# Performance work log

Hardware: AMD Instinct MI355X
Metric: run time of the kernel (lower is better)

## Reference

```python
import jax, jax.numpy as jnp
import numpy as np

D_MODEL = 256
D_CLIP = 768
NHEAD = 8
HEAD_DIM = D_MODEL // NHEAD
Q_LEN = 100
B = 32
T_LEN = 1203


def setup_inputs() -> dict:
    key = jax.random.key(0)
    ks = jax.random.split(key, 16)
    xav = lambda k, o, i: jax.random.uniform(k, (o, i), jnp.float32, -1.0, 1.0) * np.sqrt(6.0 / (o + i))
    return {
        "tgt": jax.random.normal(ks[0], (Q_LEN, B, D_MODEL), jnp.float32),
        "text_classification": jax.random.normal(ks[1], (T_LEN, D_CLIP), jnp.float32),
        "query_pos": jax.random.normal(ks[2], (Q_LEN, B, D_MODEL), jnp.float32),
        "out_of_vocab_logits": jax.random.normal(ks[3], (B, Q_LEN, T_LEN), jnp.float32),
        "Wq": xav(ks[4], D_MODEL, D_MODEL), "bq": jnp.zeros((D_MODEL,), jnp.float32),
        "Wk": xav(ks[5], D_MODEL, D_CLIP), "bk": jnp.zeros((D_MODEL,), jnp.float32),
        "Wv": xav(ks[6], D_MODEL, D_CLIP), "bv": jnp.zeros((D_MODEL,), jnp.float32),
        "Wo": xav(ks[7], D_MODEL, D_MODEL), "bo": jnp.zeros((D_MODEL,), jnp.float32),
        "ln_g": jnp.ones((D_MODEL,), jnp.float32), "ln_b": jnp.zeros((D_MODEL,), jnp.float32),
        "logit_scale": jnp.asarray(np.log(1 / 0.07), jnp.float32),
    }


def _l2norm(x, eps=1e-6):
    # F.normalize: x / max(||x||, eps)
    n = jnp.sqrt(jnp.sum(x * x, axis=-1, keepdims=True))
    return x / jnp.maximum(n, eps)


def _layernorm(x, g, b, eps=1e-5):
    mu = jnp.mean(x, axis=-1, keepdims=True)
    var = jnp.mean((x - mu) ** 2, axis=-1, keepdims=True)
    return (x - mu) * jax.lax.rsqrt(var + eps) * g + b


def reference(tgt, text_classification, query_pos, out_of_vocab_logits,
              Wq, bq, Wk, bk, Wv, bv, Wo, bo, ln_g, ln_b, logit_scale):
    qin = tgt + query_pos                       # (Q, B, d_model)
    q = qin @ Wq.T + bq                         # (Q, B, d_model)
    # text embeddings shared across batch (2D path)
    k = text_classification @ Wk.T + bk         # (T, d_model)
    v = text_classification @ Wv.T + bv         # (T, d_model)

    q = q.transpose(1, 0, 2).reshape(B, Q_LEN, NHEAD, HEAD_DIM).transpose(0, 2, 1, 3)  # (B,h,Q,hd)
    k = k.reshape(T_LEN, NHEAD, HEAD_DIM).transpose(1, 0, 2)                            # (h,T,hd)
    v = v.reshape(T_LEN, NHEAD, HEAD_DIM).transpose(1, 0, 2)                            # (h,T,hd)

    q = _l2norm(q)
    k = _l2norm(k)
    scale = jnp.minimum(jnp.exp(logit_scale), 100.0)
    in_vocab = jnp.einsum('bhqd,hkd->bhqk', q, k) * scale                                # (B,h,Q,T)

    alpha = jnp.linspace(0.0, 1.0, NHEAD, dtype=in_vocab.dtype).reshape(1, NHEAD, 1, 1)
    logits = in_vocab * (1.0 - alpha) + out_of_vocab_logits[:, None] * alpha

    attn = jax.nn.softmax(logits, axis=-1)
    out = jnp.einsum('bhqk,hkd->bhqd', attn, v)                                          # (B,h,Q,hd)
    out = out.transpose(0, 2, 1, 3).reshape(B, Q_LEN, D_MODEL).transpose(1, 0, 2)        # (Q,B,d_model)
    out = out @ Wo.T + bo

    # forward_post: residual + layernorm (dropout=0)
    return _layernorm(tgt + out, ln_g, ln_b)
```

## Files before the change

### kernel.cpp

```cpp
#include <hip/hip_runtime.h>
#include <hip/hip_bf16.h>
#include <math.h>

#define D_MODEL 256
#define D_CLIP 768
#define NHEAD 8
#define HEAD_DIM 32
#define Q_LEN 100
#define BB 32
#define T_LEN 1203
#define TPAD 1216
#define MQ (Q_LEN*BB)
#define LOG2E 1.4426950408889634f

typedef __bf16 bf16_t;
typedef __bf16 bf16x8 __attribute__((ext_vector_type(8)));
typedef __bf16 bf16x4 __attribute__((ext_vector_type(4)));
typedef float f32x4 __attribute__((ext_vector_type(4)));

static __device__ __forceinline__ bf16_t to_bf16(float x) { return (bf16_t)x; }

__global__ void prep_kernel(const float* __restrict__ tgt, const float* __restrict__ qpos,
                            const float* __restrict__ text, const float* __restrict__ Wq,
                            const float* __restrict__ Wk, const float* __restrict__ Wv,
                            const float* __restrict__ Wo,
                            bf16_t* __restrict__ qin_bf, bf16_t* __restrict__ conv_dst) {
    int idx = blockIdx.x * 256 + threadIdx.x;
    if (idx >= 566848) return;
    float4 v;
    bf16_t* dst;
    if (idx < 204800) {
        float4 a = ((const float4*)tgt)[idx];
        float4 b = ((const float4*)qpos)[idx];
        v = make_float4(a.x + b.x, a.y + b.y, a.z + b.z, a.w + b.w);
        dst = qin_bf + idx * 4;
    } else {
        int j = idx - 204800;
        const float4* src;
        if (j < 230976)      src = (const float4*)text + j;
        else if (j < 247360) src = (const float4*)Wq + (j - 230976);
        else if (j < 296512) src = (const float4*)Wk + (j - 247360);
        else if (j < 345664) src = (const float4*)Wv + (j - 296512);
        else                 src = (const float4*)Wo + (j - 345664);
        v = *src;
        dst = conv_dst + (size_t)j * 4;
    }
    bf16x4 r = { to_bf16(v.x), to_bf16(v.y), to_bf16(v.z), to_bf16(v.w) };
    *(bf16x4*)dst = r;
}

__launch_bounds__(256)
__global__ void proj_kernel(const bf16_t* __restrict__ qin_bf, const bf16_t* __restrict__ text_bf,
                            const bf16_t* __restrict__ wq, const bf16_t* __restrict__ wk,
                            const bf16_t* __restrict__ wv,
                            const float* __restrict__ bq, const float* __restrict__ bk,
                            const float* __restrict__ bv,
                            bf16_t* __restrict__ qn, bf16_t* __restrict__ kn,
                            bf16_t* __restrict__ vT) {
    const int bid = blockIdx.y;
    int z, xt;
    if (bid < 50)      { z = 0; xt = bid; }
    else if (bid < 69) { z = 1; xt = bid - 50; }
    else               { z = 2; xt = bid - 69; }
    const int j = blockIdx.x;
    const int nbase = j * 32;
    const int M = (z == 0) ? MQ : T_LEN;
    const int K = (z == 0) ? D_MODEL : D_CLIP;
    const bf16_t* W = (z == 0) ? wq : (z == 1 ? wk : wv);
    const float* bias = (z == 0) ? bq : (z == 1 ? bk : bv);

    const int wave = threadIdx.x >> 6;
    const int lane = threadIdx.x & 63;
    const int c16 = lane & 15;
    const int quad = lane >> 4;
    const int mbase = xt * 64 + wave * 16;

    f32x4 a0 = (f32x4){0.f, 0.f, 0.f, 0.f};
    f32x4 a1 = (f32x4){0.f, 0.f, 0.f, 0.f};

    const int arow = (mbase + c16 < M) ? (mbase + c16) : (M - 1);
    const bf16_t* Apb = ((z == 0) ? qin_bf : text_bf) + (size_t)arow * K + quad * 8;
    const bf16_t* W0 = W + (size_t)(nbase + c16) * K + quad * 8;
    const bf16_t* W1 = W + (size_t)(nbase + 16 + c16) * K + quad * 8;
    const int ksteps = K / 32;
    #pragma unroll 4
    for (int ks = 0; ks < ksteps; ks++) {
        bf16x8 af = *(const bf16x8*)(Apb + ks * 32);
        bf16x8 b0 = *(const bf16x8*)(W0 + ks * 32);
        bf16x8 b1 = *(const bf16x8*)(W1 + ks * 32);
        a0 = __builtin_amdgcn_mfma_f32_16x16x32_bf16(af, b0, a0, 0, 0, 0);
        a1 = __builtin_amdgcn_mfma_f32_16x16x32_bf16(af, b1, a1, 0, 0, 0);
    }

    float b0s = bias[nbase + c16];
    float b1s = bias[nbase + 16 + c16];
    #pragma unroll
    for (int r = 0; r < 4; r++) { a0[r] += b0s; a1[r] += b1s; }
    if (z < 2) {
        #pragma unroll
        for (int r = 0; r < 4; r++) {
            float s = a0[r] * a0[r] + a1[r] * a1[r];
            #pragma unroll
            for (int o = 1; o < 16; o <<= 1) s += __shfl_xor(s, o);
            float sc = 1.0f / fmaxf(sqrtf(s), 1e-6f);
            a0[r] *= sc; a1[r] *= sc;
        }
    }
    #pragma unroll
    for (int r = 0; r < 4; r++) {
        int m = mbase + quad * 4 + r;
        if (m >= M) continue;
        if (z == 0) {
            int q = m >> 5, b = m & 31;
            size_t base = ((size_t)(b * NHEAD + j) * Q_LEN + q) * HEAD_DIM;
            qn[base + c16] = to_bf16(a0[r]);
            qn[base + 16 + c16] = to_bf16(a1[r]);
        } else if (z == 1) {
            size_t base = ((size_t)j * T_LEN + m) * HEAD_DIM;
            kn[base + c16] = to_bf16(a0[r]);
            kn[base + 16 + c16] = to_bf16(a1[r]);
        } else {
            vT[(size_t)(j * 32 + c16) * TPAD + m] = to_bf16(a0[r]);
            vT[(size_t)(j * 32 + 16 + c16) * TPAD + m] = to_bf16(a1[r]);
        }
    }
}

__launch_bounds__(256)
__global__ void attn_kernel(const bf16_t* __restrict__ qn, const bf16_t* __restrict__ kn,
                            const bf16_t* __restrict__ vT, const float* __restrict__ oov,
                            const float* __restrict__ logit_scale,
                            bf16_t* __restrict__ attn_out) {
    const int b = blockIdx.x;
    const int h = blockIdx.y;
    const int qt = blockIdx.z;
    const int qbase = qt * 16;
    const int wave = threadIdx.x >> 6;
    const int lane = threadIdx.x & 63;
    const int c16 = lane & 15;
    const int quad = lane >> 4;

    __shared__ __align__(16) bf16_t p_lds[4][2][16][40];
    __shared__ float l_lds[4][16];
    __shared__ float o_lds[4][32][16];

    const float scl = fminf(expf(logit_scale[0]), 100.0f);
    const float alpha = (float)h * (1.0f / 7.0f);
    const float sscale = scl * (1.0f - alpha) * LOG2E;
    const float oscale = alpha * LOG2E;
    const float mfix = scl * (1.0f - alpha) * LOG2E + 20.0f * alpha * LOG2E;

    const int q = qbase + c16;
    const int qc = (q < Q_LEN) ? q : (Q_LEN - 1);
    bf16x8 qf = *(const bf16x8*)(qn + ((size_t)(b * NHEAD + h) * Q_LEN + qc) * HEAD_DIM + quad * 8);

    f32x4 olo = (f32x4){0.f, 0.f, 0.f, 0.f};
    f32x4 ohi = (f32x4){0.f, 0.f, 0.f, 0.f};
    float l_s = 0.0f;

    const bf16_t* knh = kn + (size_t)h * T_LEN * HEAD_DIM;
    const bf16_t* vTh = vT + (size_t)h * HEAD_DIM * TPAD;
    const float* oovr = oov + ((size_t)b * Q_LEN + qc) * T_LEN;
    const f32x4 zero = (f32x4){0.f, 0.f, 0.f, 0.f};

    for (int p = wave; p < 18; p += 4) {
        const int tb0 = p * 64;
        const int tb1 = tb0 + 32;
        bf16x8 kf00 = *(const bf16x8*)(knh + (size_t)(tb0 + c16) * HEAD_DIM + quad * 8);
        bf16x8 kf01 = *(const bf16x8*)(knh + (size_t)(tb0 + 16 + c16) * HEAD_DIM + quad * 8);
        bf16x8 kf10 = *(const bf16x8*)(knh + (size_t)(tb1 + c16) * HEAD_DIM + quad * 8);
        bf16x8 kf11 = *(const bf16x8*)(knh + (size_t)(tb1 + 16 + c16) * HEAD_DIM + quad * 8);
        float4 oa0 = *(const float4*)(oovr + tb0 + quad * 4);
        float4 oc0 = *(const float4*)(oovr + tb0 + 16 + quad * 4);
        float4 oa1 = *(const float4*)(oovr + tb1 + quad * 4);
        float4 oc1 = *(const float4*)(oovr + tb1 + 16 + quad * 4);
        bf16x8 v00 = *(const bf16x8*)(vTh + (size_t)c16 * TPAD + tb0 + quad * 8);
        bf16x8 v01 = *(const bf16x8*)(vTh + (size_t)(16 + c16) * TPAD + tb0 + quad * 8);
        bf16x8 v10 = *(const bf16x8*)(vTh + (size_t)c16 * TPAD + tb1 + quad * 8);
        bf16x8 v11 = *(const bf16x8*)(vTh + (size_t)(16 + c16) * TPAD + tb1 + quad * 8);
        f32x4 s00 = __builtin_amdgcn_mfma_f32_16x16x32_bf16(kf00, qf, zero, 0, 0, 0);
        f32x4 s01 = __builtin_amdgcn_mfma_f32_16x16x32_bf16(kf01, qf, zero, 0, 0, 0);
        f32x4 s10 = __builtin_amdgcn_mfma_f32_16x16x32_bf16(kf10, qf, zero, 0, 0, 0);
        f32x4 s11 = __builtin_amdgcn_mfma_f32_16x16x32_bf16(kf11, qf, zero, 0, 0, 0);
        float pa0[4], pc0[4], pa1[4], pc1[4];
        float ov_a0[4] = {oa0.x, oa0.y, oa0.z, oa0.w};
        float ov_c0[4] = {oc0.x, oc0.y, oc0.z, oc0.w};
        float ov_a1[4] = {oa1.x, oa1.y, oa1.z, oa1.w};
        float ov_c1[4] = {oc1.x, oc1.y, oc1.z, oc1.w};
        #pragma unroll
        for (int r = 0; r < 4; r++) {
            pa0[r] = exp2f(fmaf(s00[r], sscale, fmaf(ov_a0[r], oscale, -mfix)));
            pc0[r] = exp2f(fmaf(s01[r], sscale, fmaf(ov_c0[r], oscale, -mfix)));
            pa1[r] = exp2f(fmaf(s10[r], sscale, fmaf(ov_a1[r], oscale, -mfix)));
            pc1[r] = exp2f(fmaf(s11[r], sscale, fmaf(ov_c1[r], oscale, -mfix)));
        }
        l_s += ((pa0[0] + pa0[1]) + (pa0[2] + pa0[3])) + ((pc0[0] + pc0[1]) + (pc0[2] + pc0[3]))
             + ((pa1[0] + pa1[1]) + (pa1[2] + pa1[3])) + ((pc1[0] + pc1[1]) + (pc1[2] + pc1[3]));
        bf16x4 wA0 = { to_bf16(pa0[0]), to_bf16(pa0[1]), to_bf16(pa0[2]), to_bf16(pa0[3]) };
        bf16x4 wC0 = { to_bf16(pc0[0]), to_bf16(pc0[1]), to_bf16(pc0[2]), to_bf16(pc0[3]) };
        bf16x4 wA1 = { to_bf16(pa1[0]), to_bf16(pa1[1]), to_bf16(pa1[2]), to_bf16(pa1[3]) };
        bf16x4 wC1 = { to_bf16(pc1[0]), to_bf16(pc1[1]), to_bf16(pc1[2]), to_bf16(pc1[3]) };
        *(bf16x4*)&p_lds[wave][0][c16][quad * 4] = wA0;
        *(bf16x4*)&p_lds[wave][0][c16][16 + quad * 4] = wC0;
        *(bf16x4*)&p_lds[wave][1][c16][quad * 4] = wA1;
        *(bf16x4*)&p_lds[wave][1][c16][16 + quad * 4] = wC1;
        bf16x8 pf0 = *(const bf16x8*)(&p_lds[wave][0][c16][quad * 8]);
        bf16x8 pf1 = *(const bf16x8*)(&p_lds[wave][1][c16][quad * 8]);
        olo = __builtin_amdgcn_mfma_f32_16x16x32_bf16(v00, pf0, olo, 0, 0, 0);
        ohi = __builtin_amdgcn_mfma_f32_16x16x32_bf16(v01, pf0, ohi, 0, 0, 0);
        olo = __builtin_amdgcn_mfma_f32_16x16x32_bf16(v10, pf1, olo, 0, 0, 0);
        ohi = __builtin_amdgcn_mfma_f32_16x16x32_bf16(v11, pf1, ohi, 0, 0, 0);
    }

    if (wave == 2) {
        const int tb = 1152;
        bf16x8 kf0 = *(const bf16x8*)(knh + (size_t)(tb + c16) * HEAD_DIM + quad * 8);
        bf16x8 kf1 = *(const bf16x8*)(knh + (size_t)(tb + 16 + c16) * HEAD_DIM + quad * 8);
        float4 oa = *(const float4*)(oovr + tb + quad * 4);
        float4 oc = *(const float4*)(oovr + tb + 16 + quad * 4);
        bf16x8 v0 = *(const bf16x8*)(vTh + (size_t)c16 * TPAD + tb + quad * 8);
        bf16x8 v1 = *(const bf16x8*)(vTh + (size_t)(16 + c16) * TPAD + tb + quad * 8);
        f32x4 s0 = __builtin_amdgcn_mfma_f32_16x16x32_bf16(kf0, qf, zero, 0, 0, 0);
        f32x4 s1 = __builtin_amdgcn_mfma_f32_16x16x32_bf16(kf1, qf, zero, 0, 0, 0);
        float ova[4] = {oa.x, oa.y, oa.z, oa.w};
        float ovc[4] = {oc.x, oc.y, oc.z, oc.w};
        float p0[4], p1[4];
        #pragma unroll
        for (int r = 0; r < 4; r++) {
            p0[r] = exp2f(fmaf(s0[r], sscale, fmaf(ova[r], oscale, -mfix)));
            p1[r] = exp2f(fmaf(s1[r], sscale, fmaf(ovc[r], oscale, -mfix)));
        }
        l_s += ((p0[0] + p0[1]) + (p0[2] + p0[3])) + ((p1[0] + p1[1]) + (p1[2] + p1[3]));
        bf16x4 w0 = { to_bf16(p0[0]), to_bf16(p0[1]), to_bf16(p0[2]), to_bf16(p0[3]) };
        bf16x4 w1 = { to_bf16(p1[0]), to_bf16(p1[1]), to_bf16(p1[2]), to_bf16(p1[3]) };
        *(bf16x4*)&p_lds[wave][0][c16][quad * 4] = w0;
        *(bf16x4*)&p_lds[wave][0][c16][16 + quad * 4] = w1;
        bf16x8 pf = *(const bf16x8*)(&p_lds[wave][0][c16][quad * 8]);
        olo = __builtin_amdgcn_mfma_f32_16x16x32_bf16(v0, pf, olo, 0, 0, 0);
        ohi = __builtin_amdgcn_mfma_f32_16x16x32_bf16(v1, pf, ohi, 0, 0, 0);
    }

    if (wave == 3) {
        const int tb = 1184;
        int t1c = tb + 16 + c16;
        if (t1c >= T_LEN) t1c = T_LEN - 1;
        bf16x8 kf0 = *(const bf16x8*)(knh + (size_t)(tb + c16) * HEAD_DIM + quad * 8);
        bf16x8 kf1 = *(const bf16x8*)(knh + (size_t)t1c * HEAD_DIM + quad * 8);
        bf16x8 v0 = *(const bf16x8*)(vTh + (size_t)c16 * TPAD + tb + quad * 8);
        bf16x8 v1 = *(const bf16x8*)(vTh + (size_t)(16 + c16) * TPAD + tb + quad * 8);
        f32x4 s0 = __builtin_amdgcn_mfma_f32_16x16x32_bf16(kf0, qf, zero, 0, 0, 0);
        f32x4 s1 = __builtin_amdgcn_mfma_f32_16x16x32_bf16(kf1, qf, zero, 0, 0, 0);
        float p0[4], p1[4];
        #pragma unroll
        for (int r = 0; r < 4; r++) {
            int ta = tb + quad * 4 + r;
            int tb2 = tb + 16 + quad * 4 + r;
            float ova = oovr[ta];
            p0[r] = exp2f(fmaf(s0[r], sscale, fmaf(ova, oscale, -mfix)));
            if (tb2 < T_LEN) {
                float ovc = oovr[tb2];
                p1[r] = exp2f(fmaf(s1[r], sscale, fmaf(ovc, oscale, -mfix)));
            } else {
                p1[r] = 0.0f;
            }
        }
        l_s += ((p0[0] + p0[1]) + (p0[2] + p0[3])) + ((p1[0] + p1[1]) + (p1[2] + p1[3]));
        bf16x4 w0 = { to_bf16(p0[0]), to_bf16(p0[1]), to_bf16(p0[2]), to_bf16(p0[3]) };
        bf16x4 w1 = { to_bf16(p1[0]), to_bf16(p1[1]), to_bf16(p1[2]), to_bf16(p1[3]) };
        *(bf16x4*)&p_lds[wave][0][c16][quad * 4] = w0;
        *(bf16x4*)&p_lds[wave][0][c16][16 + quad * 4] = w1;
        bf16x8 pf = *(const bf16x8*)(&p_lds[wave][0][c16][quad * 8]);
        olo = __builtin_amdgcn_mfma_f32_16x16x32_bf16(v0, pf, olo, 0, 0, 0);
        ohi = __builtin_amdgcn_mfma_f32_16x16x32_bf16(v1, pf, ohi, 0, 0, 0);
    }

    l_s += __shfl_xor(l_s, 16);
    l_s += __shfl_xor(l_s, 32);
    if (quad == 0) l_lds[wave][c16] = l_s;
    #pragma unroll
    for (int r = 0; r < 4; r++) {
        o_lds[wave][quad * 4 + r][c16] = olo[r];
        o_lds[wave][16 + quad * 4 + r][c16] = ohi[r];
    }
    __syncthreads();
    const int q16 = threadIdx.x & 15;
    const int dd = threadIdx.x >> 4;
    float L = l_lds[0][q16] + l_lds[1][q16] + l_lds[2][q16] + l_lds[3][q16];
    const float invL = 1.0f / L;
    const int qout = qbase + q16;
    if (qout < Q_LEN) {
        #pragma unroll
        for (int half = 0; half < 2; half++) {
            int d = half * 16 + dd;
            float O = o_lds[0][d][q16] + o_lds[1][d][q16] +
                      o_lds[2][d][q16] + o_lds[3][d][q16];
            attn_out[((size_t)qout * BB + b) * D_MODEL + h * HEAD_DIM + d] = to_bf16(O * invL);
        }
    }
}

__launch_bounds__(256)
__global__ void out_kernel(const bf16_t* __restrict__ attn, const bf16_t* __restrict__ wo,
                           const float* __restrict__ bo, const float* __restrict__ tgt,
                           const float* __restrict__ ln_g, const float* __restrict__ ln_b,
                           float* __restrict__ out) {
    const int xt = blockIdx.x;
    const int wave = threadIdx.x >> 6;
    const int lane = threadIdx.x & 63;
    const int c16 = lane & 15;
    const int quad = lane >> 4;
    const int mbase = xt * 16;

    __shared__ float xs[16][264];

    f32x4 acc[4];
    #pragma unroll
    for (int i = 0; i < 4; i++) acc[i] = (f32x4){0.f, 0.f, 0.f, 0.f};
    const bf16_t* Ap = attn + (size_t)(mbase + c16) * D_MODEL + quad * 8;
    #pragma unroll
    for (int ks = 0; ks < 8; ks++) {
        bf16x8 af = *(const bf16x8*)(Ap + ks * 32);
        #pragma unroll
        for (int nt = 0; nt < 4; nt++) {
            int n = wave * 64 + nt * 16 + c16;
            bf16x8 bfr = *(const bf16x8*)(wo + (size_t)n * D_MODEL + ks * 32 + quad * 8);
            acc[nt] = __builtin_amdgcn_mfma_f32_16x16x32_bf16(af, bfr, acc[nt], 0, 0, 0);
        }
    }
    #pragma unroll
    for (int nt = 0; nt < 4; nt++) {
        int col = wave * 64 + nt * 16 + c16;
        float bb_ = bo[col];
        #pragma unroll
        for (int r = 0; r < 4; r++) {
            int m = mbase + quad * 4 + r;
            xs[quad * 4 + r][col] = acc[nt][r] + bb_ + tgt[(size_t)m * D_MODEL + col];
        }
    }
    __syncthreads();
    const int row = threadIdx.x >> 4;
    const int seg = threadIdx.x & 15;
    float sx = 0.f, sxx = 0.f;
    #pragma unroll
    for (int i = 0; i < 16; i++) {
        float x = xs[row][seg * 16 + i];
        sx += x; sxx += x * x;
    }
    #pragma unroll
    for (int o = 1; o < 16; o <<= 1) { sx += __shfl_xor(sx, o); sxx += __shfl_xor(sxx, o); }
    float mu = sx * (1.0f / 256.0f);
    float var = sxx * (1.0f / 256.0f) - mu * mu;
    float rstd = rsqrtf(fmaxf(var, 0.0f) + 1e-5f);
    size_t obase = (size_t)(mbase + row) * D_MODEL;
    #pragma unroll
    for (int i = 0; i < 16; i++) {
        int cidx = seg * 16 + i;
        out[obase + cidx] = (xs[row][cidx] - mu) * rstd * ln_g[cidx] + ln_b[cidx];
    }
}

extern "C" void kernel_launch(void* const* d_in, const int* in_sizes, int n_in,
                              void* d_out, int out_size, void* d_ws, size_t ws_size,
                              hipStream_t stream) {
    const float* tgt  = (const float*)d_in[0];
    const float* text = (const float*)d_in[1];
    const float* qpos = (const float*)d_in[2];
    const float* oov  = (const float*)d_in[3];
    const float* Wq = (const float*)d_in[4];
    const float* bq = (const float*)d_in[5];
    const float* Wk = (const float*)d_in[6];
    const float* bk = (const float*)d_in[7];
    const float* Wv = (const float*)d_in[8];
    const float* bv = (const float*)d_in[9];
    const float* Wo = (const float*)d_in[10];
    const float* bo = (const float*)d_in[11];
    const float* ln_g = (const float*)d_in[12];
    const float* ln_b = (const float*)d_in[13];
    const float* lsc  = (const float*)d_in[14];

    bf16_t* wsb = (bf16_t*)d_ws;
    bf16_t* text_bf = wsb + 0;
    bf16_t* wq_bf   = wsb + 923904;
    bf16_t* wk_bf   = wsb + 989440;
    bf16_t* wv_bf   = wsb + 1186048;
    bf16_t* wo_bf   = wsb + 1382656;
    bf16_t* qin_bf  = wsb + 1448192;
    bf16_t* qn      = wsb + 2267392;
    bf16_t* kn      = wsb + 3086592;
    bf16_t* vT      = wsb + 3394560;
    bf16_t* attn    = wsb + 3705856;
    float* out      = (float*)d_out;

    prep_kernel<<<2215, 256, 0, stream>>>(tgt, qpos, text, Wq, Wk, Wv, Wo, qin_bf, text_bf);
    proj_kernel<<<dim3(8, 88, 1), 256, 0, stream>>>(qin_bf, text_bf, wq_bf, wk_bf, wv_bf,
                                                    bq, bk, bv, qn, kn, vT);
    attn_kernel<<<dim3(32, 8, 7), 256, 0, stream>>>(qn, kn, vT, oov, lsc, attn);
    out_kernel<<<200, 256, 0, stream>>>(attn, wo_bf, bo, tgt, ln_g, ln_b, out);
}
```

Baseline: 161.0 us.

## Fuse fp32-to-bf16 conversion into GEMM loads and prefetch attention tiles

Removes the separate prep kernel that converted inputs and weights to bf16; the projection and output kernels now load fp32 directly and convert in registers, with the tgt+query_pos add fused into the Q projection. This drops one launch and a round trip of converted data through global memory, but each GEMM now reads twice the bytes per operand and repeats the conversion for every tile. The attention loop also adds software prefetching, loading the next tile's K, V and out-of-vocab data before computing the current one, which costs more registers.

After: 186.5 us. +15.8%, slower.

```diff
diff --git a/kernel.cpp b/kernel.cpp
--- a/kernel.cpp
+++ b/kernel.cpp
@@ -20,39 +20,24 @@
 
 static __device__ __forceinline__ bf16_t to_bf16(float x) { return (bf16_t)x; }
 
-__global__ void prep_kernel(const float* __restrict__ tgt, const float* __restrict__ qpos,
-                            const float* __restrict__ text, const float* __restrict__ Wq,
-                            const float* __restrict__ Wk, const float* __restrict__ Wv,
-                            const float* __restrict__ Wo,
-                            bf16_t* __restrict__ qin_bf, bf16_t* __restrict__ conv_dst) {
-    int idx = blockIdx.x * 256 + threadIdx.x;
-    if (idx >= 566848) return;
-    float4 v;
-    bf16_t* dst;
-    if (idx < 204800) {
-        float4 a = ((const float4*)tgt)[idx];
-        float4 b = ((const float4*)qpos)[idx];
-        v = make_float4(a.x + b.x, a.y + b.y, a.z + b.z, a.w + b.w);
-        dst = qin_bf + idx * 4;
-    } else {
-        int j = idx - 204800;
-        const float4* src;
-        if (j < 230976)      src = (const float4*)text + j;
-        else if (j < 247360) src = (const float4*)Wq + (j - 230976);
-        else if (j < 296512) src = (const float4*)Wk + (j - 247360);
-        else if (j < 345664) src = (const float4*)Wv + (j - 296512);
-        else                 src = (const float4*)Wo + (j - 345664);
-        v = *src;
-        dst = conv_dst + (size_t)j * 4;
-    }
-    bf16x4 r = { to_bf16(v.x), to_bf16(v.y), to_bf16(v.z), to_bf16(v.w) };
-    *(bf16x4*)dst = r;
+static __device__ __forceinline__ bf16x8 cvt8(float4 a, float4 b) {
+    bf16x8 r;
+    r[0] = to_bf16(a.x); r[1] = to_bf16(a.y); r[2] = to_bf16(a.z); r[3] = to_bf16(a.w);
+    r[4] = to_bf16(b.x); r[5] = to_bf16(b.y); r[6] = to_bf16(b.z); r[7] = to_bf16(b.w);
+    return r;
+}
+static __device__ __forceinline__ bf16x8 cvt8add(float4 a, float4 b, float4 c, float4 d) {
+    bf16x8 r;
+    r[0] = to_bf16(a.x + c.x); r[1] = to_bf16(a.y + c.y); r[2] = to_bf16(a.z + c.z); r[3] = to_bf16(a.w + c.w);
+    r[4] = to_bf16(b.x + d.x); r[5] = to_bf16(b.y + d.y); r[6] = to_bf16(b.z + d.z); r[7] = to_bf16(b.w + d.w);
+    return r;
 }
 
 __launch_bounds__(256)
-__global__ void proj_kernel(const bf16_t* __restrict__ qin_bf, const bf16_t* __restrict__ text_bf,
-                            const bf16_t* __restrict__ wq, const bf16_t* __restrict__ wk,
-                            const bf16_t* __restrict__ wv,
+__global__ void proj_kernel(const float* __restrict__ tgt, const float* __restrict__ qpos,
+                            const float* __restrict__ text,
+                            const float* __restrict__ Wq, const float* __restrict__ Wk,
+                            const float* __restrict__ Wv,
                             const float* __restrict__ bq, const float* __restrict__ bk,
                             const float* __restrict__ bv,
                             bf16_t* __restrict__ qn, bf16_t* __restrict__ kn,
@@ -66,7 +51,7 @@
     const int nbase = j * 32;
     const int M = (z == 0) ? MQ : T_LEN;
     const int K = (z == 0) ? D_MODEL : D_CLIP;
-    const bf16_t* W = (z == 0) ? wq : (z == 1 ? wk : wv);
+    const float* Wf = (z == 0) ? Wq : (z == 1 ? Wk : Wv);
     const float* bias = (z == 0) ? bq : (z == 1 ? bk : bv);
 
     const int wave = threadIdx.x >> 6;
@@ -79,17 +64,34 @@
     f32x4 a1 = (f32x4){0.f, 0.f, 0.f, 0.f};
 
     const int arow = (mbase + c16 < M) ? (mbase + c16) : (M - 1);
-    const bf16_t* Apb = ((z == 0) ? qin_bf : text_bf) + (size_t)arow * K + quad * 8;
-    const bf16_t* W0 = W + (size_t)(nbase + c16) * K + quad * 8;
-    const bf16_t* W1 = W + (size_t)(nbase + 16 + c16) * K + quad * 8;
+    const float* Ap0 = ((z == 0) ? tgt : text) + (size_t)arow * K + quad * 8;
+    const float* Ap1 = ((z == 0) ? qpos : text) + (size_t)arow * K + quad * 8;
+    const float* W0r = Wf + (size_t)(nbase + c16) * K + quad * 8;
+    const float* W1r = Wf + (size_t)(nbase + 16 + c16) * K + quad * 8;
     const int ksteps = K / 32;
-    #pragma unroll 4
-    for (int ks = 0; ks < ksteps; ks++) {
-        bf16x8 af = *(const bf16x8*)(Apb + ks * 32);
-        bf16x8 b0 = *(const bf16x8*)(W0 + ks * 32);
-        bf16x8 b1 = *(const bf16x8*)(W1 + ks * 32);
-        a0 = __builtin_amdgcn_mfma_f32_16x16x32_bf16(af, b0, a0, 0, 0, 0);
-        a1 = __builtin_amdgcn_mfma_f32_16x16x32_bf16(af, b1, a1, 0, 0, 0);
+    if (z == 0) {
+        #pragma unroll 4
+        for (int ks = 0; ks < ksteps; ks++) {
+            const int o = ks * 32;
+            float4 t0 = *(const float4*)(Ap0 + o), t1 = *(const float4*)(Ap0 + o + 4);
+            float4 p0 = *(const float4*)(Ap1 + o), p1 = *(const float4*)(Ap1 + o + 4);
+            float4 w00 = *(const float4*)(W0r + o), w01 = *(const float4*)(W0r + o + 4);
+            float4 w10 = *(const float4*)(W1r + o), w11 = *(const float4*)(W1r + o + 4);
+            bf16x8 af = cvt8add(t0, t1, p0, p1);
+            a0 = __builtin_amdgcn_mfma_f32_16x16x32_bf16(af, cvt8(w00, w01), a0, 0, 0, 0);
+            a1 = __builtin_amdgcn_mfma_f32_16x16x32_bf16(af, cvt8(w10, w11), a1, 0, 0, 0);
+        }
+    } else {
+        #pragma unroll 4
+        for (int ks = 0; ks < ksteps; ks++) {
+            const int o = ks * 32;
+            float4 t0 = *(const float4*)(Ap0 + o), t1 = *(const float4*)(Ap0 + o + 4);
+            float4 w00 = *(const float4*)(W0r + o), w01 = *(const float4*)(W0r + o + 4);
+            float4 w10 = *(const float4*)(W1r + o), w11 = *(const float4*)(W1r + o + 4);
+            bf16x8 af = cvt8(t0, t1);
+            a0 = __builtin_amdgcn_mfma_f32_16x16x32_bf16(af, cvt8(w00, w01), a0, 0, 0, 0);
+            a1 = __builtin_amdgcn_mfma_f32_16x16x32_bf16(af, cvt8(w10, w11), a1, 0, 0, 0);
+        }
     }
 
     float b0s = bias[nbase + c16];
@@ -148,7 +150,7 @@
     const float alpha = (float)h * (1.0f / 7.0f);
     const float sscale = scl * (1.0f - alpha) * LOG2E;
     const float oscale = alpha * LOG2E;
-    const float mfix = scl * (1.0f - alpha) * LOG2E + 20.0f * alpha * LOG2E;
+    const float mfix = sscale + 20.0f * oscale;
 
     const int q = qbase + c16;
     const int qc = (q < Q_LEN) ? q : (Q_LEN - 1);
@@ -163,54 +165,70 @@
     const float* oovr = oov + ((size_t)b * Q_LEN + qc) * T_LEN;
     const f32x4 zero = (f32x4){0.f, 0.f, 0.f, 0.f};
 
+    bf16x8 kA0, kA1, kB0, kB1, vA0, vA1, vB0, vB1;
+    float4 oA0, oA1, oB0, oB1;
+
+    #define LOAD_PAIR(P, kA0_, kA1_, kB0_, kB1_, vA0_, vA1_, vB0_, vB1_, oA0_, oA1_, oB0_, oB1_) \
+        { const int tb0_ = (P) * 64; const int tb1_ = tb0_ + 32;                                   \
+          kA0_ = *(const bf16x8*)(knh + (size_t)(tb0_ + c16) * HEAD_DIM + quad * 8);               \
+          kA1_ = *(const bf16x8*)(knh + (size_t)(tb0_ + 16 + c16) * HEAD_DIM + quad * 8);          \
+          kB0_ = *(const bf16x8*)(knh + (size_t)(tb1_ + c16) * HEAD_DIM + quad * 8);               \
+          kB1_ = *(const bf16x8*)(knh + (size_t)(tb1_ + 16 + c16) * HEAD_DIM + quad * 8);          \
+          vA0_ = *(const bf16x8*)(vTh + (size_t)c16 * TPAD + tb0_ + quad * 8);                     \
+          vA1_ = *(const bf16x8*)(vTh + (size_t)(16 + c16) * TPAD + tb0_ + quad * 8);              \
+          vB0_ = *(const bf16x8*)(vTh + (size_t)c16 * TPAD + tb1_ + quad * 8);                     \
+          vB1_ = *(const bf16x8*)(vTh + (size_t)(16 + c16) * TPAD + tb1_ + quad * 8);              \
+          oA0_ = *(const float4*)(oovr + tb0_ + quad * 4);                                         \
+          oA1_ = *(const float4*)(oovr + tb0_ + 16 + quad * 4);                                    \
+          oB0_ = *(const float4*)(oovr + tb1_ + quad * 4);                                         \
+          oB1_ = *(const float4*)(oovr + tb1_ + 16 + quad * 4); }
+
+    if (wave < 18) LOAD_PAIR(wave, kA0, kA1, kB0, kB1, vA0, vA1, vB0, vB1, oA0, oA1, oB0, oB1);
+
     for (int p = wave; p < 18; p += 4) {
-        const int tb0 = p * 64;
-        const int tb1 = tb0 + 32;
-        bf16x8 kf00 = *(const bf16x8*)(knh + (size_t)(tb0 + c16) * HEAD_DIM + quad * 8);
-        bf16x8 kf01 = *(const bf16x8*)(knh + (size_t)(tb0 + 16 + c16) * HEAD_DIM + quad * 8);
-        bf16x8 kf10 = *(const bf16x8*)(knh + (size_t)(tb1 + c16) * HEAD_DIM + quad * 8);
-        bf16x8 kf11 = *(const bf16x8*)(knh + (size_t)(tb1 + 16 + c16) * HEAD_DIM + quad * 8);
-        float4 oa0 = *(const float4*)(oovr + tb0 + quad * 4);
-        float4 oc0 = *(const float4*)(oovr + tb0 + 16 + quad * 4);
-        float4 oa1 = *(const float4*)(oovr + tb1 + quad * 4);
-        float4 oc1 = *(const float4*)(oovr + tb1 + 16 + quad * 4);
-        bf16x8 v00 = *(const bf16x8*)(vTh + (size_t)c16 * TPAD + tb0 + quad * 8);
-        bf16x8 v01 = *(const bf16x8*)(vTh + (size_t)(16 + c16) * TPAD + tb0 + quad * 8);
-        bf16x8 v10 = *(const bf16x8*)(vTh + (size_t)c16 * TPAD + tb1 + quad * 8);
-        bf16x8 v11 = *(const bf16x8*)(vTh + (size_t)(16 + c16) * TPAD + tb1 + quad * 8);
-        f32x4 s00 = __builtin_amdgcn_mfma_f32_16x16x32_bf16(kf00, qf, zero, 0, 0, 0);
-        f32x4 s01 = __builtin_amdgcn_mfma_f32_16x16x32_bf16(kf01, qf, zero, 0, 0, 0);
-        f32x4 s10 = __builtin_amdgcn_mfma_f32_16x16x32_bf16(kf10, qf, zero, 0, 0, 0);
-        f32x4 s11 = __builtin_amdgcn_mfma_f32_16x16x32_bf16(kf11, qf, zero, 0, 0, 0);
-        float pa0[4], pc0[4], pa1[4], pc1[4];
-        float ov_a0[4] = {oa0.x, oa0.y, oa0.z, oa0.w};
-        float ov_c0[4] = {oc0.x, oc0.y, oc0.z, oc0.w};
-        float ov_a1[4] = {oa1.x, oa1.y, oa1.z, oa1.w};
-        float ov_c1[4] = {oc1.x, oc1.y, oc1.z, oc1.w};
+        const int pn = (p + 4 < 18) ? (p + 4) : 17;
+        bf16x8 nkA0, nkA1, nkB0, nkB1, nvA0, nvA1, nvB0, nvB1;
+        float4 noA0, noA1, noB0, noB1;
+        LOAD_PAIR(pn, nkA0, nkA1, nkB0, nkB1, nvA0, nvA1, nvB0, nvB1, noA0, noA1, noB0, noB1);
+
+        f32x4 s00 = __builtin_amdgcn_mfma_f32_16x16x32_bf16(kA0, qf, zero, 0, 0, 0);
+        f32x4 s01 = __builtin_amdgcn_mfma_f32_16x16x32_bf16(kA1, qf, zero, 0, 0, 0);
+        f32x4 s10 = __builtin_amdgcn_mfma_f32_16x16x32_bf16(kB0, qf, zero, 0, 0, 0);
+        f32x4 s11 = __builtin_amdgcn_mfma_f32_16x16x32_bf16(kB1, qf, zero, 0, 0, 0);
+        float pa0[4], pa1[4], pb0[4], pb1[4];
+        float ovA0[4] = {oA0.x, oA0.y, oA0.z, oA0.w};
+        float ovA1[4] = {oA1.x, oA1.y, oA1.z, oA1.w};
+        float ovB0[4] = {oB0.x, oB0.y, oB0.z, oB0.w};
+        float ovB1[4] = {oB1.x, oB1.y, oB1.z, oB1.w};
         #pragma unroll
         for (int r = 0; r < 4; r++) {
-            pa0[r] = exp2f(fmaf(s00[r], sscale, fmaf(ov_a0[r], oscale, -mfix)));
-            pc0[r] = exp2f(fmaf(s01[r], sscale, fmaf(ov_c0[r], oscale, -mfix)));
-            pa1[r] = exp2f(fmaf(s10[r], sscale, fmaf(ov_a1[r], oscale, -mfix)));
-            pc1[r] = exp2f(fmaf(s11[r], sscale, fmaf(ov_c1[r], oscale, -mfix)));
-        }
-        l_s += ((pa0[0] + pa0[1]) + (pa0[2] + pa0[3])) + ((pc0[0] + pc0[1]) + (pc0[2] + pc0[3]))
-             + ((pa1[0] + pa1[1]) + (pa1[2] + pa1[3])) + ((pc1[0] + pc1[1]) + (pc1[2] + pc1[3]));
+            pa0[r] = exp2f(fmaf(s00[r], sscale, fmaf(ovA0[r], oscale, -mfix)));
+            pa1[r] = exp2f(fmaf(s01[r], sscale, fmaf(ovA1[r], oscale, -mfix)));
+            pb0[r] = exp2f(fmaf(s10[r], sscale, fmaf(ovB0[r], oscale, -mfix)));
+            pb1[r] = exp2f(fmaf(s11[r], sscale, fmaf(ovB1[r], oscale, -mfix)));
+        }
+        l_s += ((pa0[0] + pa0[1]) + (pa0[2] + pa0[3])) + ((pa1[0] + pa1[1]) + (pa1[2] + pa1[3]))
+             + ((pb0[0] + pb0[1]) + (pb0[2] + pb0[3])) + ((pb1[0] + pb1[1]) + (pb1[2] + pb1[3]));
         bf16x4 wA0 = { to_bf16(pa0[0]), to_bf16(pa0[1]), to_bf16(pa0[2]), to_bf16(pa0[3]) };
-        bf16x4 wC0 = { to_bf16(pc0[0]), to_bf16(pc0[1]), to_bf16(pc0[2]), to_bf16(pc0[3]) };
         bf16x4 wA1 = { to_bf16(pa1[0]), to_bf16(pa1[1]), to_bf16(pa1[2]), to_bf16(pa1[3]) };
-        bf16x4 wC1 = { to_bf16(pc1[0]), to_bf16(pc1[1]), to_bf16(pc1[2]), to_bf16(pc1[3]) };
+        bf16x4 wB0 = { to_bf16(pb0[0]), to_bf16(pb0[1]), to_bf16(pb0[2]), to_bf16(pb0[3]) };
+        bf16x4 wB1 = { to_bf16(pb1[0]), to_bf16(pb1[1]), to_bf16(pb1[2]), to_bf16(pb1[3]) };
         *(bf16x4*)&p_lds[wave][0][c16][quad * 4] = wA0;
-        *(bf16x4*)&p_lds[wave][0][c16][16 + quad * 4] = wC0;
-        *(bf16x4*)&p_lds[wave][1][c16][quad * 4] = wA1;
-        *(bf16x4*)&p_lds[wave][1][c16][16 + quad * 4] = wC1;
+        *(bf16x4*)&p_lds[wave][0][c16][16 + quad * 4] = wA1;
+        *(bf16x4*)&p_lds[wave][1][c16][quad * 4] = wB0;
+        *(bf16x4*)&p_lds[wave][1][c16][16 + quad * 4] = wB1;
         bf16x8 pf0 = *(const bf16x8*)(&p_lds[wave][0][c16][quad * 8]);
         bf16x8 pf1 = *(const bf16x8*)(&p_lds[wave][1][c16][quad * 8]);
-        olo = __builtin_amdgcn_mfma_f32_16x16x32_bf16(v00, pf0, olo, 0, 0, 0);
-        ohi = __builtin_amdgcn_mfma_f32_16x16x32_bf16(v01, pf0, ohi, 0, 0, 0);
-        olo = __builtin_amdgcn_mfma_f32_16x16x32_bf16(v10, pf1, olo, 0, 0, 0);
-        ohi = __builtin_amdgcn_mfma_f32_16x16x32_bf16(v11, pf1, ohi, 0, 0, 0);
-    }
+        olo = __builtin_amdgcn_mfma_f32_16x16x32_bf16(vA0, pf0, olo, 0, 0, 0);
+        ohi = __builtin_amdgcn_mfma_f32_16x16x32_bf16(vA1, pf0, ohi, 0, 0, 0);
+        olo = __builtin_amdgcn_mfma_f32_16x16x32_bf16(vB0, pf1, olo, 0, 0, 0);
+        ohi = __builtin_amdgcn_mfma_f32_16x16x32_bf16(vB1, pf1, ohi, 0, 0, 0);
+
+        kA0 = nkA0; kA1 = nkA1; kB0 = nkB0; kB1 = nkB1;
+        vA0 = nvA0; vA1 = nvA1; vB0 = nvB0; vB1 = nvB1;
+        oA0 = noA0; oA1 = noA1; oB0 = noB0; oB1 = noB1;
+    }
+    #undef LOAD_PAIR
 
     if (wave == 2) {
         const int tb = 1152;
@@ -300,7 +318,7 @@
 }
 
 __launch_bounds__(256)
-__global__ void out_kernel(const bf16_t* __restrict__ attn, const bf16_t* __restrict__ wo,
+__global__ void out_kernel(const bf16_t* __restrict__ attn, const float* __restrict__ Wo,
                            const float* __restrict__ bo, const float* __restrict__ tgt,
                            const float* __restrict__ ln_g, const float* __restrict__ ln_b,
                            float* __restrict__ out) {
@@ -323,8 +341,10 @@
         #pragma unroll
         for (int nt = 0; nt < 4; nt++) {
             int n = wave * 64 + nt * 16 + c16;
-            bf16x8 bfr = *(const bf16x8*)(wo + (size_t)n * D_MODEL + ks * 32 + quad * 8);
-            acc[nt] = __builtin_amdgcn_mfma_f32_16x16x32_bf16(af, bfr, acc[nt], 0, 0, 0);
+            const float* wr = Wo + (size_t)n * D_MODEL + ks * 32 + quad * 8;
+            float4 w0 = *(const float4*)wr;
+            float4 w1 = *(const float4*)(wr + 4);
+            acc[nt] = __builtin_amdgcn_mfma_f32_16x16x32_bf16(af, cvt8(w0, w1), acc[nt], 0, 0, 0);
         }
     }
     #pragma unroll
@@ -379,21 +399,14 @@
     const float* lsc  = (const float*)d_in[14];
 
     bf16_t* wsb = (bf16_t*)d_ws;
-    bf16_t* text_bf = wsb + 0;
-    bf16_t* wq_bf   = wsb + 923904;
-    bf16_t* wk_bf   = wsb + 989440;
-    bf16_t* wv_bf   = wsb + 1186048;
-    bf16_t* wo_bf   = wsb + 1382656;
-    bf16_t* qin_bf  = wsb + 1448192;
-    bf16_t* qn      = wsb + 2267392;
-    bf16_t* kn      = wsb + 3086592;
-    bf16_t* vT      = wsb + 3394560;
-    bf16_t* attn    = wsb + 3705856;
-    float* out      = (float*)d_out;
-
-    prep_kernel<<<2215, 256, 0, stream>>>(tgt, qpos, text, Wq, Wk, Wv, Wo, qin_bf, text_bf);
-    proj_kernel<<<dim3(8, 88, 1), 256, 0, stream>>>(qin_bf, text_bf, wq_bf, wk_bf, wv_bf,
+    bf16_t* qn   = wsb + 0;
+    bf16_t* kn   = wsb + 819200;
+    bf16_t* vT   = wsb + 1127168;
+    bf16_t* attn = wsb + 1438464;
+    float* out   = (float*)d_out;
+
+    proj_kernel<<<dim3(8, 88, 1), 256, 0, stream>>>(tgt, qpos, text, Wq, Wk, Wv,
                                                     bq, bk, bv, qn, kn, vT);
     attn_kernel<<<dim3(32, 8, 7), 256, 0, stream>>>(qn, kn, vT, oov, lsc, attn);
-    out_kernel<<<200, 256, 0, stream>>>(attn, wo_bf, bo, tgt, ln_g, ln_b, out);
-}
+    out_kernel<<<200, 256, 0, stream>>>(attn, Wo, bo, tgt, ln_g, ln_b, out);
+}
```
